# Optimization experiments

Measured on AMD Instinct MI355X. Metric: run time of the kernel, lower is better.

## Reference

```python
import jax, jax.numpy as jnp
import numpy as np

C = 96        # dim
HEADS = 8     # FrameHistoryRouter heads (StateAlignBlock forces heads=1)
WS = 4        # window_size = 2*scale_patchsize
NFC = 1       # num_frames_tocache
TOPK = 5
LOCAL_N = 4


def conv(x, w, stride=1, pad=0, groups=1):
    return jax.lax.conv_general_dilated(
        x, w, (stride, stride), [(pad, pad), (pad, pad)],
        dimension_numbers=("NCHW", "OIHW", "NCHW"), feature_group_count=groups)


def l2norm(x, axis):
    n = jnp.linalg.norm(x, axis=axis, keepdims=True)
    return x / jnp.maximum(n, 1e-12)


def setup_inputs() -> dict:
    key = jax.random.key(0)
    ks = jax.random.split(key, 16)
    def rn(i, shp, s=0.02):
        return jax.random.normal(ks[i], shp, dtype=jnp.float32) * s
    return {
        "x": jax.random.normal(ks[0], (2, C, 256, 256), dtype=jnp.float32),
        "sab_qk_w": rn(1, (2 * C, C, 1, 1)),
        "sab_qk_dw": rn(2, (2 * C, 1, 3, 3)),
        "sab_v_w": rn(3, (C, C, 1, 1)),
        "sab_v_dw": rn(4, (C, 1, 3, 3)),
        "sab_k2_w": rn(5, (2 * C, C, 1, 1)),
        "sab_k2_dw": rn(6, (2 * C, 1, WS, WS)),
        "sab_q2_w": rn(7, (2 * C, C, 1, 1)),
        "sab_q2_dw": rn(8, (2 * C, 1, WS, WS)),
        "sab_proj_w": rn(9, (C, C, 1, 1)),
        "sab_temp": jnp.ones((1, 1, 1), jnp.float32),
        "fhr_qkv_w": rn(10, (3 * C, C, 1, 1)),
        "fhr_qkv_dw": rn(11, (3 * C, 1, 3, 3)),
        "fhr_proj_w": rn(12, (C, C, 1, 1)),
        "fhr_temp": jnp.ones((HEADS, 1, 1), jnp.float32),
    }


def _forward(x, sab_qk_w, sab_qk_dw, sab_v_w, sab_v_dw, sab_k2_w, sab_k2_dw,
             sab_q2_w, sab_q2_dw, sab_proj_w, sab_temp,
             fhr_qkv_w, fhr_qkv_dw, fhr_proj_w, fhr_temp):
    b, c, h, w = x.shape
    # ---------- StateAlignBlock (no cache: first frame) ----------
    qk = conv(conv(x, sab_qk_w), sab_qk_dw, pad=1, groups=2 * c)
    q, k = jnp.split(qk, 2, axis=1)
    v = conv(conv(x, sab_v_w), sab_v_dw, pad=1, groups=c)
    k = conv(conv(k, sab_k2_w), sab_k2_dw, stride=WS, pad=1, groups=2 * c)
    q = conv(conv(q, sab_q2_w), sab_q2_dw, stride=WS, pad=1, groups=2 * c)
    H, W = q.shape[2], q.shape[3]            # = h//WS, w//WS
    N = H * W
    # b (1 d) h w -> b 1 1 (h w) d   with d = 2c
    q = q.reshape(b, 2 * c, N).transpose(0, 2, 1)[:, None, None]
    k = k.reshape(b, 2 * c, N).transpose(0, 2, 1)[:, None, None]
    # v: b (1 d) (p1 h) (p2 w) -> b 1 1 (h w) (p1 p2 d), p1=p2=WS, d=c
    h2, w2 = h // WS, w // WS
    v = v.reshape(b, c, WS, h2, WS, w2).transpose(0, 3, 5, 2, 4, 1)
    v = v.reshape(b, 1, 1, h2 * w2, WS * WS * c)
    q = l2norm(q, -1)
    k = l2norm(k, -1)
    attn = jnp.einsum("bfgnd,bfgmd->bfgnm", q, k) * sab_temp  # [b,1,1,N,N]
    # zero_out_non_top_k (top-5 along last dim; threshold form, ties negligible)
    kth = jax.lax.top_k(attn, TOPK)[0][..., TOPK - 1:TOPK]
    topk_mask = (attn >= kth).astype(attn.dtype)
    # local attention mask: manhattan distance <= LOCAL_N on the HxW patch grid
    yy, xx = jnp.meshgrid(jnp.arange(H), jnp.arange(W), indexing="ij")
    coords = jnp.stack([yy.ravel(), xx.ravel()], axis=-1)          # [N,2]
    dist = jnp.abs(coords[:, None, :] - coords[None, :, :]).sum(-1)
    local = (dist <= LOCAL_N).astype(attn.dtype)                   # [N,N]
    attn = attn * topk_mask + attn * local                         # as in torch
    # clipped_softmax
    zero = attn == 0
    s = jax.nn.softmax(jnp.where(zero, -jnp.inf, attn), axis=-1)
    s = jnp.where(zero, 0.0, s)
    s = s / s.sum(-1, keepdims=True)
    out = jnp.einsum("bfgnm,bfgmd->bfgnd", s, v)  # [b,1,1,N, WS*WS*c]
    F = 1  # curr_num_frames (no cache)
    # b f 1 (h w) (p1 p2 d) -> (b f) d (p1 h) (p2 w)
    out = out.reshape(b * F, h2, w2, WS, WS, c).transpose(0, 5, 3, 1, 4, 2)
    out = out.reshape(b * F, c, h, w)
    out = conv(out, sab_proj_w)
    aligned = out.reshape(b, F, c, h, w)
    k_s = k[:, -NFC:]  # [b,1,1,N,2c]
    v_s = v[:, -NFC:]
    # ---------- FrameHistoryRouter on aligned current frame ----------
    x2 = aligned[:, -1]
    qkv = conv(conv(x2, fhr_qkv_w), fhr_qkv_dw, pad=1, groups=3 * c)
    q2, k2, v2 = jnp.split(qkv, 3, axis=1)
    hd = c // HEADS
    q2 = q2.reshape(b, HEADS, hd, h * w)
    k2 = k2.reshape(b, HEADS, hd, h * w)
    v2 = v2.reshape(b, HEADS, hd, h * w)
    q2 = l2norm(q2, -1)
    k2 = l2norm(k2, -1)
    a2 = jnp.einsum("bhcn,bhdn->bhcd", q2, k2) * fhr_temp  # [b,H,hd,hd]
    a2 = jax.nn.softmax(a2, axis=-1)
    o2 = jnp.einsum("bhcd,bhdn->bhcn", a2, v2).reshape(b, c, h, w)
    o2 = conv(o2, fhr_proj_w)
    keep = int(NFC * c / HEADS)  # = hd
    return o2, k_s, v_s, k2[:, :, -keep:, :], v2[:, :, -keep:, :]


def reference(x, sab_qk_w, sab_qk_dw, sab_v_w, sab_v_dw, sab_k2_w, sab_k2_dw,
              sab_q2_w, sab_q2_dw, sab_proj_w, sab_temp,
              fhr_qkv_w, fhr_qkv_dw, fhr_proj_w, fhr_temp):
    return _forward(x, sab_qk_w, sab_qk_dw, sab_v_w, sab_v_dw, sab_k2_w,
                    sab_k2_dw, sab_q2_w, sab_q2_dw, sab_proj_w, sab_temp,
                    fhr_qkv_w, fhr_qkv_dw, fhr_proj_w, fhr_temp)
```

## Files before the change

### kernel.cpp

```cpp
#include <hip/hip_runtime.h>
#include <hip/hip_bf16.h>
#include <math.h>

#define HW 65536L

typedef __attribute__((ext_vector_type(8))) short bf16x8;
typedef __attribute__((ext_vector_type(4))) float f32x4;

__device__ __forceinline__ int iabs_(int v) { return v < 0 ? -v : v; }

__global__ __launch_bounds__(256) void wsplit(
    const float* __restrict__ qk, const float* __restrict__ v,
    const float* __restrict__ q2, const float* __restrict__ k2,
    const float* __restrict__ pj, const float* __restrict__ fq,
    const float* __restrict__ fp, unsigned short* __restrict__ whl)
{
  const int e = blockIdx.x*256 + threadIdx.x;
  if (e >= 110592) return;
  const int row = e / 96, col = e - row*96;
  float f;
  if      (row <  192) f = qk[e];
  else if (row <  288) f = v [(row-192)*96+col];
  else if (row <  480) f = q2[(row-288)*96+col];
  else if (row <  672) f = k2[(row-480)*96+col];
  else if (row <  768) f = pj[(row-672)*96+col];
  else if (row < 1056) f = fq[(row-768)*96+col];
  else                 f = fp[(row-1056)*96+col];
  __hip_bfloat16 h = __float2bfloat16(f);
  float hf = __bfloat162float(h);
  __hip_bfloat16 l = __float2bfloat16(f - hf);
  whl[e]          = *(unsigned short*)&h;
  whl[110592 + e] = *(unsigned short*)&l;
}

#define BLDS 104
__global__ __launch_bounds__(256) void conv1x1_mfma(
    const float* __restrict__ in, long in_bstride,
    const unsigned short* __restrict__ whl, int wrow0,
    float* __restrict__ out, long out_bstride,
    int mtiles, int mode)
{
  __shared__ unsigned short bhs[128*BLDS];
  __shared__ unsigned short bls[128*BLDS];
  const int t = threadIdx.x;
  const int p0 = blockIdx.x * 128;
  const int b = blockIdx.y;
  if (mode == 0) {
    #pragma unroll
    for (int it = 0; it < 48; it++) {
      const int idx = it*256 + t;
      const int c = idx >> 7, pix = idx & 127;
      float f = in[(long)b*in_bstride + (long)c*HW + p0 + pix];
      __hip_bfloat16 h = __float2bfloat16(f);
      float hf = __bfloat162float(h);
      __hip_bfloat16 l = __float2bfloat16(f - hf);
      bhs[pix*BLDS + c] = *(unsigned short*)&h;
      bls[pix*BLDS + c] = *(unsigned short*)&l;
    }
  } else {
    const int pp = t >> 1, half = (t & 1)*48;
    const int p = p0 + pp;
    const int py = p >> 8, px = p & 255;
    const float* src = in + (long)b*in_bstride
        + ((long)((py & 63)*64 + (px & 63))*16 + ((py >> 6)*4 + (px >> 6)))*96 + half;
    #pragma unroll
    for (int j4 = 0; j4 < 12; j4++) {
      float4 v4 = *(const float4*)&src[j4*4];
      float fv[4] = {v4.x, v4.y, v4.z, v4.w};
      #pragma unroll
      for (int u = 0; u < 4; u++) {
        __hip_bfloat16 h = __float2bfloat16(fv[u]);
        float hf = __bfloat162float(h);
        __hip_bfloat16 l = __float2bfloat16(fv[u] - hf);
        bhs[pp*BLDS + half + j4*4 + u] = *(unsigned short*)&h;
        bls[pp*BLDS + half + j4*4 + u] = *(unsigned short*)&l;
      }
    }
  }
  __syncthreads();
  const int lane = t & 63, w = t >> 6;
  const int fr = lane & 15, fk = lane >> 4;
  bf16x8 Bh[2][3], Bl[2][3];
  #pragma unroll
  for (int nt = 0; nt < 2; nt++)
    #pragma unroll
    for (int kt = 0; kt < 3; kt++) {
      const int pix = w*32 + nt*16 + fr;
      Bh[nt][kt] = *(const bf16x8*)(bhs + pix*BLDS + kt*32 + fk*8);
      Bl[nt][kt] = *(const bf16x8*)(bls + pix*BLDS + kt*32 + fk*8);
    }
  float* dst = out + (long)b*out_bstride + p0 + w*32;
  for (int m = 0; m < mtiles; m++) {
    const long wbase = (long)(wrow0 + m*16 + fr)*96 + fk*8;
    bf16x8 Ah[3], Al[3];
    #pragma unroll
    for (int kt = 0; kt < 3; kt++) {
      Ah[kt] = *(const bf16x8*)(whl + wbase + kt*32);
      Al[kt] = *(const bf16x8*)(whl + 110592 + wbase + kt*32);
    }
    f32x4 acc[2] = {};
    #pragma unroll
    for (int nt = 0; nt < 2; nt++)
      #pragma unroll
      for (int kt = 0; kt < 3; kt++) {
        acc[nt] = __builtin_amdgcn_mfma_f32_16x16x32_bf16(Ah[kt], Bh[nt][kt], acc[nt], 0, 0, 0);
        acc[nt] = __builtin_amdgcn_mfma_f32_16x16x32_bf16(Ah[kt], Bl[nt][kt], acc[nt], 0, 0, 0);
        acc[nt] = __builtin_amdgcn_mfma_f32_16x16x32_bf16(Al[kt], Bh[nt][kt], acc[nt], 0, 0, 0);
      }
    #pragma unroll
    for (int nt = 0; nt < 2; nt++)
      #pragma unroll
      for (int r = 0; r < 4; r++)
        dst[(long)(m*16 + fk*4 + r)*HW + nt*16 + fr] = acc[nt][r];
  }
}

__global__ __launch_bounds__(256) void dw3x3v(
    const float* __restrict__ in, const float* __restrict__ w,
    float* __restrict__ out, int CH)
{
  const int t = threadIdx.x;
  const int p4 = blockIdx.x * 256 + t;
  const int ch = blockIdx.y, b = blockIdx.z;
  const int y = p4 >> 6, x0 = (p4 & 63) << 2;
  const float* ip = in + (long)(b*CH + ch) * HW;
  const float* wp = w + ch*9;
  float a0 = 0.f, a1 = 0.f, a2 = 0.f, a3 = 0.f;
  #pragma unroll
  for (int dy = -1; dy <= 1; dy++) {
    const int yy = y + dy;
    if (yy < 0 || yy > 255) continue;
    const float* rp = ip + yy*256;
    const float4 c = *(const float4*)&rp[x0];
    const float left  = (x0 > 0)   ? rp[x0-1] : 0.f;
    const float right = (x0 < 252) ? rp[x0+4] : 0.f;
    const float w0 = wp[(dy+1)*3+0], w1 = wp[(dy+1)*3+1], w2 = wp[(dy+1)*3+2];
    a0 = fmaf(left, w0, a0); a0 = fmaf(c.x, w1, a0); a0 = fmaf(c.y, w2, a0);
    a1 = fmaf(c.x,  w0, a1); a1 = fmaf(c.y, w1, a1); a1 = fmaf(c.z, w2, a1);
    a2 = fmaf(c.y,  w0, a2); a2 = fmaf(c.z, w1, a2); a2 = fmaf(c.w, w2, a2);
    a3 = fmaf(c.z,  w0, a3); a3 = fmaf(c.w, w1, a3); a3 = fmaf(right, w2, a3);
  }
  float4 o; o.x = a0; o.y = a1; o.z = a2; o.w = a3;
  *(float4*)&out[(long)(b*CH + ch)*HW + y*256 + x0] = o;
}

__global__ __launch_bounds__(256) void dw3x3_vs(
    const float* __restrict__ in, const float* __restrict__ w,
    float* __restrict__ vs)
{
  __shared__ float tile[96*65];
  const int t = threadIdx.x;
  const int gb = blockIdx.x;
  const int b = blockIdx.y;
  const int y = gb >> 2, xb = gb & 3;
  #pragma unroll
  for (int i = 0; i < 6; i++) {
    const int idx = i*256 + t;
    const int ci = idx >> 4, q = idx & 15;
    const int x0 = xb*64 + q*4;
    const float* ip = in + ((long)b*96 + ci) * HW;
    const float* wp = w + ci*9;
    float a0 = 0.f, a1 = 0.f, a2 = 0.f, a3 = 0.f;
    #pragma unroll
    for (int dy = -1; dy <= 1; dy++) {
      const int yy = y + dy;
      if (yy < 0 || yy > 255) continue;
      const float* rp = ip + yy*256;
      const float4 c = *(const float4*)&rp[x0];
      const float left  = (x0 > 0)   ? rp[x0-1] : 0.f;
      const float right = (x0 < 252) ? rp[x0+4] : 0.f;
      const float w0 = wp[(dy+1)*3+0], w1 = wp[(dy+1)*3+1], w2 = wp[(dy+1)*3+2];
      a0 = fmaf(left, w0, a0); a0 = fmaf(c.x, w1, a0); a0 = fmaf(c.y, w2, a0);
      a1 = fmaf(c.x,  w0, a1); a1 = fmaf(c.y, w1, a1); a1 = fmaf(c.z, w2, a1);
      a2 = fmaf(c.y,  w0, a2); a2 = fmaf(c.z, w1, a2); a2 = fmaf(c.w, w2, a2);
      a3 = fmaf(c.z,  w0, a3); a3 = fmaf(c.w, w1, a3); a3 = fmaf(right, w2, a3);
    }
    const int xl = q*4;
    tile[ci*65 + xl    ] = a0;
    tile[ci*65 + xl + 1] = a1;
    tile[ci*65 + xl + 2] = a2;
    tile[ci*65 + xl + 3] = a3;
  }
  __syncthreads();
  const int blk = (y >> 6)*4 + xb;
  float* obase = vs + ((long)b*4096 + (long)(y & 63)*64) * 1536 + blk*96;
  #pragma unroll
  for (int i = 0; i < 24; i++) {
    const int idx = i*256 + t;
    const int nl = idx / 96, ci = idx % 96;
    obase[(long)nl*1536 + ci] = tile[ci*65 + nl];
  }
}

__global__ __launch_bounds__(256) void dw4x4s4(
    const float* __restrict__ in, const float* __restrict__ w,
    float* __restrict__ out)
{
  const int t = threadIdx.x;
  const int op = blockIdx.x * 256 + t;
  const int ch = blockIdx.y, b = blockIdx.z;
  const int oy = op >> 6, ox = op & 63;
  const float* ip = in + (long)(b*192 + ch) * HW;
  const float* wp = w + ch*16;
  float acc = 0.f;
  #pragma unroll
  for (int ty = 0; ty < 4; ty++) {
    int iy = 4*oy + ty - 1;
    if (iy < 0 || iy > 255) continue;
    #pragma unroll
    for (int tx = 0; tx < 4; tx++) {
      int ix = 4*ox + tx - 1;
      if (ix < 0 || ix > 255) continue;
      acc = fmaf(ip[iy*256 + ix], wp[ty*4 + tx], acc);
    }
  }
  out[(long)(b*192 + ch) * 4096 + op] = acc;
}

__global__ __launch_bounds__(256) void l2n192(
    const float* __restrict__ in, float* __restrict__ out)
{
  const int t = threadIdx.x;
  const int wid = t >> 6, lane = t & 63;
  const int gw = blockIdx.x * 4 + wid;
  const int b = gw >> 12, n = gw & 4095;
  const float* ip = in + (long)b * 786432;
  float v0 = ip[(long)(lane      ) * 4096 + n];
  float v1 = ip[(long)(lane +  64) * 4096 + n];
  float v2 = ip[(long)(lane + 128) * 4096 + n];
  float ss = v0*v0 + v1*v1 + v2*v2;
  #pragma unroll
  for (int s = 1; s < 64; s <<= 1) ss += __shfl_xor(ss, s, 64);
  float nrm = fmaxf(sqrtf(ss), 1e-12f);
  float* op = out + ((long)b*4096 + n) * 192;
  op[lane      ] = v0 / nrm;
  op[lane +  64] = v1 / nrm;
  op[lane + 128] = v2 / nrm;
}

__global__ __launch_bounds__(256) void bf16split(
    const float* __restrict__ in, unsigned short* __restrict__ outp)
{
  const int i = blockIdx.x * 256 + threadIdx.x;
  const int n = i / 192, k = i % 192;
  float f = in[i];
  __hip_bfloat16 h = __float2bfloat16(f);
  float hf = __bfloat162float(h);
  __hip_bfloat16 l = __float2bfloat16(f - hf);
  outp[(long)n*384 + k]       = *(unsigned short*)&h;
  outp[(long)n*384 + 192 + k] = *(unsigned short*)&l;
}

#define LDSROW 40
__global__ __launch_bounds__(256) void attn_qk_mfma(
    const unsigned short* __restrict__ Qsp, const unsigned short* __restrict__ Ksp,
    float* __restrict__ attn, const float* __restrict__ tp)
{
  __shared__ unsigned short qs[256*LDSROW];
  __shared__ unsigned short ks[256*LDSROW];
  const int t = threadIdx.x;
  const int lane = t & 63, w = t >> 6;
  const int n0 = blockIdx.x * 128;
  const int m0 = blockIdx.y * 128;
  const int wr = (w >> 1) * 64, wc = (w & 1) * 64;
  f32x4 acc[4][4] = {};
  const int srow = t & 127;
  const int shl  = t >> 7;
  const unsigned short* qsrc = Qsp + (long)(n0 + srow) * 384 + shl * 192;
  const unsigned short* ksrc = Ksp + (long)(m0 + srow) * 384 + shl * 192;
  unsigned short* qdst = qs + (shl*128 + srow) * LDSROW;
  unsigned short* kdst = ks + (shl*128 + srow) * LDSROW;
  const int fr = lane & 15;
  const int fk = lane >> 4;
  for (int s = 0; s < 6; s++) {
    __syncthreads();
    #pragma unroll
    for (int j = 0; j < 4; j++) {
      *(bf16x8*)(qdst + j*8) = *(const bf16x8*)(qsrc + s*32 + j*8);
      *(bf16x8*)(kdst + j*8) = *(const bf16x8*)(ksrc + s*32 + j*8);
    }
    __syncthreads();
    bf16x8 ah[4], al[4], bh[4], bl[4];
    #pragma unroll
    for (int i = 0; i < 4; i++) {
      ah[i] = *(const bf16x8*)(qs + (      wr + i*16 + fr) * LDSROW + fk*8);
      al[i] = *(const bf16x8*)(qs + (128 + wr + i*16 + fr) * LDSROW + fk*8);
      bh[i] = *(const bf16x8*)(ks + (      wc + i*16 + fr) * LDSROW + fk*8);
      bl[i] = *(const bf16x8*)(ks + (128 + wc + i*16 + fr) * LDSROW + fk*8);
    }
    #pragma unroll
    for (int i = 0; i < 4; i++)
      #pragma unroll
      for (int j = 0; j < 4; j++) {
        acc[i][j] = __builtin_amdgcn_mfma_f32_16x16x32_bf16(ah[i], bh[j], acc[i][j], 0, 0, 0);
        acc[i][j] = __builtin_amdgcn_mfma_f32_16x16x32_bf16(ah[i], bl[j], acc[i][j], 0, 0, 0);
        acc[i][j] = __builtin_amdgcn_mfma_f32_16x16x32_bf16(al[i], bh[j], acc[i][j], 0, 0, 0);
      }
  }
  const float temp = tp[0];
  #pragma unroll
  for (int i = 0; i < 4; i++)
    #pragma unroll
    for (int j = 0; j < 4; j++)
      #pragma unroll
      for (int r = 0; r < 4; r++) {
        const int nn = n0 + wr + i*16 + (lane >> 4)*4 + r;
        const int mm = m0 + wc + j*16 + (lane & 15);
        attn[(long)nn*4096 + mm] = acc[i][j][r] * temp;
      }
}

#define CAP 128
__global__ __launch_bounds__(256) void attn_out_k(
    const float* __restrict__ attn, const float* __restrict__ vs,
    float* __restrict__ outr)
{
  __shared__ float row[4096];
  __shared__ float top5[256*5];
  __shared__ int   lm[CAP];
  __shared__ float lw[CAP];
  __shared__ float ses[CAP];
  __shared__ float redf[8];
  __shared__ int   scan[256];
  const int t = threadIdx.x;
  const int n = blockIdx.x;
  const float* ar = attn + (long)n * 4096;
  #pragma unroll
  for (int k = 0; k < 16; k++) row[k*256 + t] = ar[k*256 + t];
  __syncthreads();
  float t0=-INFINITY,t1=-INFINITY,t2=-INFINITY,t3=-INFINITY,t4=-INFINITY;
  #pragma unroll
  for (int k = 0; k < 16; k++) {
    float v = row[k*256 + t];
    if (v > t4) {
      if (v > t0)      { t4=t3; t3=t2; t2=t1; t1=t0; t0=v; }
      else if (v > t1) { t4=t3; t3=t2; t2=t1; t1=v; }
      else if (v > t2) { t4=t3; t3=t2; t2=v; }
      else if (v > t3) { t4=t3; t3=v; }
      else             { t4=v; }
    }
  }
  top5[t*5+0]=t0; top5[t*5+1]=t1; top5[t*5+2]=t2; top5[t*5+3]=t3; top5[t*5+4]=t4;
  __syncthreads();
  for (int s = 128; s >= 1; s >>= 1) {
    if (t < s) {
      float* A = &top5[t*5];
      const float* B = &top5[(t+s)*5];
      float m[5]; int i = 0, j = 0;
      #pragma unroll
      for (int k = 0; k < 5; k++) {
        float av = A[i], bv = B[j];
        if (av >= bv) { m[k] = av; i++; } else { m[k] = bv; j++; }
      }
      #pragma unroll
      for (int k = 0; k < 5; k++) A[k] = m[k];
    }
    __syncthreads();
  }
  const float kth = top5[4];
  const int y = n >> 6, x = n & 63;
  int myc = 0;
  float wmax = -INFINITY;
  #pragma unroll
  for (int k = 0; k < 16; k++) {
    int m = k*256 + t;
    float a = row[m];
    int c = ((a >= kth) ? 1 : 0) +
            (((iabs_(y - (m >> 6)) + iabs_(x - (m & 63))) <= 4) ? 1 : 0);
    float wv = a * (float)c;
    if (wv != 0.0f) { myc++; wmax = fmaxf(wmax, wv); }
  }
  scan[t] = myc;
  __syncthreads();
  for (int s = 1; s < 256; s <<= 1) {
    int v = (t >= s) ? scan[t-s] : 0;
    __syncthreads();
    scan[t] += v;
    __syncthreads();
  }
  const int base = scan[t] - myc;
  const int cnt = scan[255];
  {
    int idx = base;
    #pragma unroll
    for (int k = 0; k < 16; k++) {
      int m = k*256 + t;
      float a = row[m];
      int c = ((a >= kth) ? 1 : 0) +
              (((iabs_(y - (m >> 6)) + iabs_(x - (m & 63))) <= 4) ? 1 : 0);
      float wv = a * (float)c;
      if (wv != 0.0f && idx < CAP) { lm[idx] = m; lw[idx] = wv; idx++; }
    }
  }
  #pragma unroll
  for (int s = 1; s < 64; s <<= 1) wmax = fmaxf(wmax, __shfl_xor(wmax, s, 64));
  if ((t & 63) == 0) redf[t >> 6] = wmax;
  __syncthreads();
  const float gmax = fmaxf(fmaxf(redf[0], redf[1]), fmaxf(redf[2], redf[3]));
  __syncthreads();
  if (t < cnt && t < CAP) ses[t] = expf(lw[t] - gmax);
  __syncthreads();
  float ps = (t < cnt && t < CAP) ? ses[t] : 0.f;
  #pragma unroll
  for (int s = 1; s < 64; s <<= 1) ps += __shfl_xor(ps, s, 64);
  if ((t & 63) == 0) redf[4 + (t >> 6)] = ps;
  __syncthreads();
  const float S = redf[4] + redf[5] + redf[6] + redf[7];
  const float invS = 1.0f / S;
  float a0=0,a1=0,a2=0,a3=0,a4=0,a5=0;
  const int ecnt = (cnt < CAP) ? cnt : CAP;
  for (int e = 0; e < ecnt; e++) {
    float se = ses[e] * invS;
    const float* vr = vs + (long)lm[e] * 1536;
    a0 = fmaf(se, vr[        t], a0);
    a1 = fmaf(se, vr[ 256 + t], a1);
    a2 = fmaf(se, vr[ 512 + t], a2);
    a3 = fmaf(se, vr[ 768 + t], a3);
    a4 = fmaf(se, vr[1024 + t], a4);
    a5 = fmaf(se, vr[1280 + t], a5);
  }
  float* orow = outr + (long)n * 1536;
  orow[        t] = a0;
  orow[ 256 + t] = a1;
  orow[ 512 + t] = a2;
  orow[ 768 + t] = a3;
  orow[1024 + t] = a4;
  orow[1280 + t] = a5;
}

__global__ __launch_bounds__(1024) void l2n_sp(
    const float* __restrict__ in, float* __restrict__ out)
{
  const int ch = blockIdx.x, b = blockIdx.y, t = threadIdx.x;
  const float* ip = in + ((long)b*96 + ch) * HW;
  float ss = 0.f;
  for (int i = t; i < 65536; i += 1024) { float v = ip[i]; ss = fmaf(v, v, ss); }
  __shared__ float red[16];
  #pragma unroll
  for (int s = 1; s < 64; s <<= 1) ss += __shfl_xor(ss, s, 64);
  if ((t & 63) == 0) red[t >> 6] = ss;
  __syncthreads();
  if (t == 0) {
    float s2 = 0.f;
    for (int i = 0; i < 16; i++) s2 += red[i];
    red[0] = fmaxf(sqrtf(s2), 1e-12f);
  }
  __syncthreads();
  const float nrm = red[0];
  float* op = out + ((long)b*96 + ch) * HW;
  for (int i = t; i < 65536; i += 1024) op[i] = ip[i] / nrm;
}

#define A2_NCH 16
__global__ __launch_bounds__(256) void a2_part(
    const float* __restrict__ q2n, const float* __restrict__ k2n,
    float* __restrict__ part)
{
  __shared__ float sh[24*260];
  const int t = threadIdx.x;
  const int ch = blockIdx.x, h = blockIdx.y, b = blockIdx.z;
  const long base = ((long)b*96 + h*12) * HW + ch*4096;
  const int c = t / 12, d = t - (t/12)*12;
  float acc = 0.f;
  for (int sub = 0; sub < 16; sub++) {
    __syncthreads();
    #pragma unroll
    for (int j = 0; j < 6; j++) {
      const int v = j*256 + t;
      const int row = v >> 6;
      const int col4 = v & 63;
      const float* src = (row < 12)
        ? q2n + base + (long)row*HW + sub*256 + col4*4
        : k2n + base + (long)(row-12)*HW + sub*256 + col4*4;
      *(float4*)&sh[row*260 + col4*4] = *(const float4*)src;
    }
    __syncthreads();
    if (t < 144) {
      const float* qr = &sh[c*260];
      const float* kr = &sh[(12+d)*260];
      #pragma unroll
      for (int i4 = 0; i4 < 64; i4++) {
        float4 qv = *(const float4*)&qr[i4*4];
        float4 kv = *(const float4*)&kr[i4*4];
        acc = fmaf(qv.x, kv.x, acc);
        acc = fmaf(qv.y, kv.y, acc);
        acc = fmaf(qv.z, kv.z, acc);
        acc = fmaf(qv.w, kv.w, acc);
      }
    }
  }
  if (t < 144)
    part[(((long)b*8 + h)*A2_NCH + ch)*144 + t] = acc;
}

__global__ __launch_bounds__(256) void a2_fin(
    const float* __restrict__ part, const float* __restrict__ temp,
    float* __restrict__ a2s)
{
  __shared__ float m[144];
  const int t = threadIdx.x;
  const int h = blockIdx.x, b = blockIdx.y;
  if (t < 144) {
    float s = 0.f;
    const float* pp = part + (((long)b*8 + h)*A2_NCH)*144 + t;
    #pragma unroll
    for (int ch = 0; ch < A2_NCH; ch++) s += pp[ch*144];
    m[t] = s * temp[h];
  }
  __syncthreads();
  if (t < 12) {
    float mx = -INFINITY;
    #pragma unroll
    for (int d = 0; d < 12; d++) mx = fmaxf(mx, m[t*12+d]);
    float e[12], sum = 0.f;
    #pragma unroll
    for (int d = 0; d < 12; d++) { e[d] = expf(m[t*12+d]-mx); sum += e[d]; }
    float inv = 1.0f/sum;
    float* op = a2s + (((long)b*8 + h)*12 + t)*12;
    #pragma unroll
    for (int d = 0; d < 12; d++) op[d] = e[d]*inv;
  }
}

__global__ __launch_bounds__(256) void o2pre_kern(
    const float* __restrict__ a2s, const float* __restrict__ v2,
    float* __restrict__ o2p)
{
  const int t = threadIdx.x;
  const int n = blockIdx.x * 256 + t;
  const int bh = blockIdx.y, b = bh >> 3, h = bh & 7;
  const float* a = a2s + (long)bh * 144;
  const float* vb = v2 + ((long)b*96 + h*12) * HW;
  float vv[12];
  #pragma unroll
  for (int d = 0; d < 12; d++) vv[d] = vb[(long)d*HW + n];
  float* ob = o2p + ((long)b*96 + h*12) * HW;
  #pragma unroll
  for (int c = 0; c < 12; c++) {
    float s = 0.f;
    #pragma unroll
    for (int d = 0; d < 12; d++) s = fmaf(a[c*12 + d], vv[d], s);
    ob[(long)c*HW + n] = s;
  }
}

extern "C" void kernel_launch(void* const* d_in, const int* in_sizes, int n_in,
                              void* d_out, int out_size, void* d_ws, size_t ws_size,
                              hipStream_t stream) {
  const float* x        = (const float*)d_in[0];
  const float* qk_w     = (const float*)d_in[1];
  const float* qk_dw    = (const float*)d_in[2];
  const float* v_w      = (const float*)d_in[3];
  const float* v_dw     = (const float*)d_in[4];
  const float* k2_w     = (const float*)d_in[5];
  const float* k2_dw    = (const float*)d_in[6];
  const float* q2_w     = (const float*)d_in[7];
  const float* q2_dw    = (const float*)d_in[8];
  const float* proj_w   = (const float*)d_in[9];
  const float* sab_temp = (const float*)d_in[10];
  const float* fqkv_w   = (const float*)d_in[11];
  const float* fqkv_dw  = (const float*)d_in[12];
  const float* fproj_w  = (const float*)d_in[13];
  const float* fhr_temp = (const float*)d_in[14];
  float* out = (float*)d_out;
  float* ws  = (float*)d_ws;

  float* O2  = out;
  float* KS  = out + 12582912;
  float* VS  = out + 14155776;
  float* K2N = out + 26738688;
  float* V2  = out + 39321600;

  float* A0   = ws;
  float* A1   = ws + 25165824;
  float* QD   = ws + 50331648;
  float* KD   = ws + 51904512;
  float* QN   = ws + 53477376;
  float* A2S  = ws + 55050240;
  float* PART = ws + 55052544;
  unsigned short* QSP = (unsigned short*)(A0 + 16777216);
  unsigned short* KSP = (unsigned short*)(A0 + 16777216 + 786432);
  unsigned short* WHL = (unsigned short*)QN;

  dim3 b256(256), b1024(1024);

  wsplit<<<dim3(432), b256, 0, stream>>>(qk_w, v_w, q2_w, k2_w, proj_w, fqkv_w, fproj_w, WHL);
  conv1x1_mfma<<<dim3(512,2), b256, 0, stream>>>(x, 96L*HW, WHL, 0, A0, 192L*HW, 12, 0);
  dw3x3v<<<dim3(64,192,2), b256, 0, stream>>>(A0, qk_dw, A1, 192);
  conv1x1_mfma<<<dim3(512,2), b256, 0, stream>>>(x, 96L*HW, WHL, 192, A0, 96L*HW, 6, 0);
  dw3x3_vs<<<dim3(1024,2), b256, 0, stream>>>(A0, v_dw, VS);
  conv1x1_mfma<<<dim3(512,2), b256, 0, stream>>>(A1, 192L*HW, WHL, 288, A0, 192L*HW, 12, 0);
  dw4x4s4<<<dim3(16,192,2), b256, 0, stream>>>(A0, q2_dw, QD);
  conv1x1_mfma<<<dim3(512,2), b256, 0, stream>>>(A1 + 96L*HW, 192L*HW, WHL, 480, A0, 192L*HW, 12, 0);
  dw4x4s4<<<dim3(16,192,2), b256, 0, stream>>>(A0, k2_dw, KD);
  l2n192<<<dim3(2048), b256, 0, stream>>>(QD, QN);
  l2n192<<<dim3(2048), b256, 0, stream>>>(KD, KS);
  for (int b = 0; b < 2; b++) {
    bf16split<<<dim3(3072), b256, 0, stream>>>(QN + (long)b*786432, QSP);
    bf16split<<<dim3(3072), b256, 0, stream>>>(KS + (long)b*786432, KSP);
    attn_qk_mfma<<<dim3(32,32), b256, 0, stream>>>(QSP, KSP, A0, sab_temp);
    attn_out_k<<<dim3(4096), b256, 0, stream>>>(
        A0, VS + (long)b*6291456, A1 + (long)b*6291456);
  }
  wsplit<<<dim3(432), b256, 0, stream>>>(qk_w, v_w, q2_w, k2_w, proj_w, fqkv_w, fproj_w, WHL);
  conv1x1_mfma<<<dim3(512,2), b256, 0, stream>>>(A1, 6291456L, WHL, 672, A0, 96L*HW, 6, 1);
  float* PRE  = A0 + 12582912;
  float* DW1  = A1 + 12582912;
  float* Q2NB = A1;
  conv1x1_mfma<<<dim3(512,2), b256, 0, stream>>>(A0, 96L*HW, WHL, 768, PRE, 96L*HW, 6, 0);
  dw3x3v<<<dim3(64,96,2), b256, 0, stream>>>(PRE, fqkv_dw,        DW1, 96);
  l2n_sp<<<dim3(96,2), b1024, 0, stream>>>(DW1, Q2NB);
  conv1x1_mfma<<<dim3(512,2), b256, 0, stream>>>(A0, 96L*HW, WHL, 864, PRE, 96L*HW, 6, 0);
  dw3x3v<<<dim3(64,96,2), b256, 0, stream>>>(PRE, fqkv_dw +  864, DW1, 96);
  l2n_sp<<<dim3(96,2), b1024, 0, stream>>>(DW1, K2N);
  conv1x1_mfma<<<dim3(512,2), b256, 0, stream>>>(A0, 96L*HW, WHL, 960, PRE, 96L*HW, 6, 0);
  dw3x3v<<<dim3(64,96,2), b256, 0, stream>>>(PRE, fqkv_dw + 1728, V2, 96);
  a2_part<<<dim3(A2_NCH,8,2), b256, 0, stream>>>(Q2NB, K2N, PART);
  a2_fin<<<dim3(8,2), b256, 0, stream>>>(PART, fhr_temp, A2S);
  o2pre_kern<<<dim3(256,16), b256, 0, stream>>>(A2S, V2, A0);
  conv1x1_mfma<<<dim3(512,2), b256, 0, stream>>>(A0, 96L*HW, WHL, 1056, O2, 96L*HW, 6, 0);
}
```

Measured before the change: 918.2 us.

## Fuse FHR qkv 1x1 convs into one pass and vectorize bf16 split staging

The three separate 96-channel 1x1 convolutions for the FrameHistoryRouter q/k/v are merged into one conv1x1_mfma launch producing 288 channels. The aligned input is then staged to LDS once instead of three times, and two launches are removed. The depthwise kernel gains separate input/output channel strides so it can read from the 288-channel buffer. The bf16 hi/lo split now truncates bits to get the high half and writes four packed values per LDS store instead of one scalar short each, cutting conversion work and LDS store count. In-place l2norm and a reshuffled workspace layout trade extra buffer aliasing care for fewer passes over the input.

```diff
diff --git a/kernel.cpp b/kernel.cpp
--- a/kernel.cpp
+++ b/kernel.cpp
@@ -47,15 +47,26 @@
   const int b = blockIdx.y;
   if (mode == 0) {
     #pragma unroll
-    for (int it = 0; it < 48; it++) {
+    for (int it = 0; it < 12; it++) {
       const int idx = it*256 + t;
-      const int c = idx >> 7, pix = idx & 127;
-      float f = in[(long)b*in_bstride + (long)c*HW + p0 + pix];
-      __hip_bfloat16 h = __float2bfloat16(f);
-      float hf = __bfloat162float(h);
-      __hip_bfloat16 l = __float2bfloat16(f - hf);
-      bhs[pix*BLDS + c] = *(unsigned short*)&h;
-      bls[pix*BLDS + c] = *(unsigned short*)&l;
+      const int g = idx >> 7;
+      const int pix = idx & 127;
+      const float* src = in + (long)b*in_bstride + (long)(g*4)*HW + p0 + pix;
+      unsigned hh[4], ll[4];
+      #pragma unroll
+      for (int j = 0; j < 4; j++) {
+        float f = src[(long)j*HW];
+        unsigned u = __float_as_uint(f);
+        hh[j] = u >> 16;
+        float lof = f - __uint_as_float(u & 0xFFFF0000u);
+        __hip_bfloat16 lb = __float2bfloat16(lof);
+        ll[j] = *(unsigned short*)&lb;
+      }
+      uint2 hv, lv;
+      hv.x = hh[0] | (hh[1] << 16); hv.y = hh[2] | (hh[3] << 16);
+      lv.x = ll[0] | (ll[1] << 16); lv.y = ll[2] | (ll[3] << 16);
+      *(uint2*)(bhs + pix*BLDS + g*4) = hv;
+      *(uint2*)(bls + pix*BLDS + g*4) = lv;
     }
   } else {
     const int pp = t >> 1, half = (t & 1)*48;
@@ -67,14 +78,20 @@
     for (int j4 = 0; j4 < 12; j4++) {
       float4 v4 = *(const float4*)&src[j4*4];
       float fv[4] = {v4.x, v4.y, v4.z, v4.w};
-      #pragma unroll
-      for (int u = 0; u < 4; u++) {
-        __hip_bfloat16 h = __float2bfloat16(fv[u]);
-        float hf = __bfloat162float(h);
-        __hip_bfloat16 l = __float2bfloat16(fv[u] - hf);
-        bhs[pp*BLDS + half + j4*4 + u] = *(unsigned short*)&h;
-        bls[pp*BLDS + half + j4*4 + u] = *(unsigned short*)&l;
+      unsigned hh[4], ll[4];
+      #pragma unroll
+      for (int u4 = 0; u4 < 4; u4++) {
+        unsigned u = __float_as_uint(fv[u4]);
+        hh[u4] = u >> 16;
+        float lof = fv[u4] - __uint_as_float(u & 0xFFFF0000u);
+        __hip_bfloat16 lb = __float2bfloat16(lof);
+        ll[u4] = *(unsigned short*)&lb;
       }
+      uint2 hv, lv;
+      hv.x = hh[0] | (hh[1] << 16); hv.y = hh[2] | (hh[3] << 16);
+      lv.x = ll[0] | (ll[1] << 16); lv.y = ll[2] | (ll[3] << 16);
+      *(uint2*)(bhs + pp*BLDS + half + j4*4) = hv;
+      *(uint2*)(bls + pp*BLDS + half + j4*4) = lv;
     }
   }
   __syncthreads();
@@ -116,14 +133,14 @@
 }
 
 __global__ __launch_bounds__(256) void dw3x3v(
-    const float* __restrict__ in, const float* __restrict__ w,
-    float* __restrict__ out, int CH)
+    const float* __restrict__ in, int inCH, const float* __restrict__ w,
+    float* __restrict__ out, int outCH)
 {
   const int t = threadIdx.x;
   const int p4 = blockIdx.x * 256 + t;
   const int ch = blockIdx.y, b = blockIdx.z;
   const int y = p4 >> 6, x0 = (p4 & 63) << 2;
-  const float* ip = in + (long)(b*CH + ch) * HW;
+  const float* ip = in + ((long)b*inCH + ch) * HW;
   const float* wp = w + ch*9;
   float a0 = 0.f, a1 = 0.f, a2 = 0.f, a3 = 0.f;
   #pragma unroll
@@ -141,7 +158,7 @@
     a3 = fmaf(c.z,  w0, a3); a3 = fmaf(c.w, w1, a3); a3 = fmaf(right, w2, a3);
   }
   float4 o; o.x = a0; o.y = a1; o.z = a2; o.w = a3;
-  *(float4*)&out[(long)(b*CH + ch)*HW + y*256 + x0] = o;
+  *(float4*)&out[((long)b*outCH + ch)*HW + y*256 + x0] = o;
 }
 
 __global__ __launch_bounds__(256) void dw3x3_vs(
@@ -581,12 +598,15 @@
   unsigned short* QSP = (unsigned short*)(A0 + 16777216);
   unsigned short* KSP = (unsigned short*)(A0 + 16777216 + 786432);
   unsigned short* WHL = (unsigned short*)QN;
+  float* ALN = ws;
+  float* PRE = ws + 12582912;
+  float* OB  = ws + 12582912;
 
   dim3 b256(256), b1024(1024);
 
   wsplit<<<dim3(432), b256, 0, stream>>>(qk_w, v_w, q2_w, k2_w, proj_w, fqkv_w, fproj_w, WHL);
   conv1x1_mfma<<<dim3(512,2), b256, 0, stream>>>(x, 96L*HW, WHL, 0, A0, 192L*HW, 12, 0);
-  dw3x3v<<<dim3(64,192,2), b256, 0, stream>>>(A0, qk_dw, A1, 192);
+  dw3x3v<<<dim3(64,192,2), b256, 0, stream>>>(A0, 192, qk_dw, A1, 192);
   conv1x1_mfma<<<dim3(512,2), b256, 0, stream>>>(x, 96L*HW, WHL, 192, A0, 96L*HW, 6, 0);
   dw3x3_vs<<<dim3(1024,2), b256, 0, stream>>>(A0, v_dw, VS);
   conv1x1_mfma<<<dim3(512,2), b256, 0, stream>>>(A1, 192L*HW, WHL, 288, A0, 192L*HW, 12, 0);
@@ -603,20 +623,15 @@
         A0, VS + (long)b*6291456, A1 + (long)b*6291456);
   }
   wsplit<<<dim3(432), b256, 0, stream>>>(qk_w, v_w, q2_w, k2_w, proj_w, fqkv_w, fproj_w, WHL);
-  conv1x1_mfma<<<dim3(512,2), b256, 0, stream>>>(A1, 6291456L, WHL, 672, A0, 96L*HW, 6, 1);
-  float* PRE  = A0 + 12582912;
-  float* DW1  = A1 + 12582912;
-  float* Q2NB = A1;
-  conv1x1_mfma<<<dim3(512,2), b256, 0, stream>>>(A0, 96L*HW, WHL, 768, PRE, 96L*HW, 6, 0);
-  dw3x3v<<<dim3(64,96,2), b256, 0, stream>>>(PRE, fqkv_dw,        DW1, 96);
-  l2n_sp<<<dim3(96,2), b1024, 0, stream>>>(DW1, Q2NB);
-  conv1x1_mfma<<<dim3(512,2), b256, 0, stream>>>(A0, 96L*HW, WHL, 864, PRE, 96L*HW, 6, 0);
-  dw3x3v<<<dim3(64,96,2), b256, 0, stream>>>(PRE, fqkv_dw +  864, DW1, 96);
-  l2n_sp<<<dim3(96,2), b1024, 0, stream>>>(DW1, K2N);
-  conv1x1_mfma<<<dim3(512,2), b256, 0, stream>>>(A0, 96L*HW, WHL, 960, PRE, 96L*HW, 6, 0);
-  dw3x3v<<<dim3(64,96,2), b256, 0, stream>>>(PRE, fqkv_dw + 1728, V2, 96);
-  a2_part<<<dim3(A2_NCH,8,2), b256, 0, stream>>>(Q2NB, K2N, PART);
+  conv1x1_mfma<<<dim3(512,2), b256, 0, stream>>>(A1, 6291456L, WHL, 672, ALN, 96L*HW, 6, 1);
+  conv1x1_mfma<<<dim3(512,2), b256, 0, stream>>>(ALN, 96L*HW, WHL, 768, PRE, 288L*HW, 18, 0);
+  dw3x3v<<<dim3(64,96,2), b256, 0, stream>>>(PRE,            288, fqkv_dw,        ALN, 96);
+  dw3x3v<<<dim3(64,96,2), b256, 0, stream>>>(PRE +  96L*HW, 288, fqkv_dw +  864, K2N, 96);
+  dw3x3v<<<dim3(64,96,2), b256, 0, stream>>>(PRE + 192L*HW, 288, fqkv_dw + 1728, V2,  96);
+  l2n_sp<<<dim3(96,2), b1024, 0, stream>>>(ALN, ALN);
+  l2n_sp<<<dim3(96,2), b1024, 0, stream>>>(K2N, K2N);
+  a2_part<<<dim3(A2_NCH,8,2), b256, 0, stream>>>(ALN, K2N, PART);
   a2_fin<<<dim3(8,2), b256, 0, stream>>>(PART, fhr_temp, A2S);
-  o2pre_kern<<<dim3(256,16), b256, 0, stream>>>(A2S, V2, A0);
-  conv1x1_mfma<<<dim3(512,2), b256, 0, stream>>>(A0, 96L*HW, WHL, 1056, O2, 96L*HW, 6, 0);
-}
+  o2pre_kern<<<dim3(256,16), b256, 0, stream>>>(A2S, V2, OB);
+  conv1x1_mfma<<<dim3(512,2), b256, 0, stream>>>(OB, 96L*HW, WHL, 1056, O2, 96L*HW, 6, 0);
+}
```

Result: no change. 903.5 us (-1.6%).
